# Kernel optimization log

Measured on AMD Instinct MI355X. Metric: run time of the kernel, lower is better.

The kernel has to match this reference:

```python
import jax, jax.numpy as jnp
import numpy as np


def setup_inputs() -> dict:
    key = jax.random.key(0)
    ks = jax.random.split(key, 5)
    b, t, q_dim, kv_dim, h = 16, 128, 256, 64, 4
    c = t - 1
    q_x = jax.random.normal(ks[0], (b, t, q_dim), dtype=jnp.float32)
    kv_x = jax.random.normal(ks[1], (b, t, c, kv_dim), dtype=jnp.float32)
    # Linear weights stored as [in, out]; no biases (bias=False in torch module).
    sq = 1.0 / np.sqrt(q_dim)
    sk = 1.0 / np.sqrt(kv_dim)
    Wq = jax.random.uniform(ks[2], (q_dim, kv_dim * h), jnp.float32, -sq, sq)
    Wk = jax.random.uniform(ks[3], (kv_dim, kv_dim * h), jnp.float32, -sk, sk)
    Wv = jax.random.uniform(ks[4], (kv_dim, kv_dim * h), jnp.float32, -sk, sk)
    return {"q_x": q_x, "kv_x": kv_x, "Wq": Wq, "Wk": Wk, "Wv": Wv}


def reference(q_x, kv_x, Wq, Wk, Wv):
    b, t, c, k = kv_x.shape  # c = t - 1
    h = Wq.shape[1] // k
    # projections
    q = (q_x @ Wq).reshape(b, t, h, k)          # [b,t,h,k]
    keys = (kv_x @ Wk).reshape(b, t, c, h, k)   # [b,t,c,h,k]
    vals = (kv_x @ Wv).reshape(b, t, c, h, k)
    # per-token attention over the c-sized context
    scores = jnp.einsum('bthk,btchk->bthc', q, keys) / jnp.sqrt(jnp.float32(k))
    w = jax.nn.softmax(scores, axis=-1)          # softmax over context dim
    out = jnp.einsum('bthc,btchk->bthk', w, vals)
    return out.reshape(b, t, h * k)
```

## Files before the change

### kernel.cpp

```cpp
#include <hip/hip_runtime.h>
#include <math.h>

#define Bdim 16
#define Tdim 128
#define Cdim 127
#define Hdim 4
#define QD   256
#define HK   256
#define BT   (Bdim * Tdim)

#define DPP_XOR1 0xB1
#define DPP_XOR2 0x4E
template<int CTRL>
__device__ __forceinline__ float dpp_movf(float x) {
    return __int_as_float(__builtin_amdgcn_update_dpp(
        0, __float_as_int(x), CTRL, 0xF, 0xF, true));
}
__device__ __forceinline__ float dot4(float4 a, float4 b, float s) {
    return fmaf(a.x, b.x, fmaf(a.y, b.y, fmaf(a.z, b.z, fmaf(a.w, b.w, s))));
}
__device__ __forceinline__ float4 fma4(float e, float4 x, float4 v) {
    v.x = fmaf(e, x.x, v.x); v.y = fmaf(e, x.y, v.y);
    v.z = fmaf(e, x.z, v.z); v.w = fmaf(e, x.w, v.w);
    return v;
}
__device__ __forceinline__ float4 add4(float4 a, float4 b) {
    return make_float4(a.x + b.x, a.y + b.y, a.z + b.z, a.w + b.w);
}
__device__ __forceinline__ float4 shfl4(float4 v, int m) {
    return make_float4(__shfl_xor(v.x, m, 64), __shfl_xor(v.y, m, 64),
                       __shfl_xor(v.z, m, 64), __shfl_xor(v.w, m, 64));
}
__device__ __forceinline__ float4 sel4(int c, float4 a, float4 b) {
    return c ? a : b;
}

__global__ __launch_bounds__(256) void qk_fused(
        const float* __restrict__ q_x,
        const float* __restrict__ Wq,
        const float* __restrict__ Wk,
        float* __restrict__ qk) {
    __shared__ __align__(16) float q_s[4][256];
    __shared__ __align__(16) float p_s[4][4][68];
    int RB = blockIdx.x;
    int tid = threadIdx.x;
    {
        int r = tid >> 6, kq = tid & 63;
        *(float4*)&q_s[r][kq*4] =
            *(const float4*)(q_x + (size_t)(RB*4 + r) * QD + kq * 4);
    }
    __syncthreads();

    float acc[4] = {0.f, 0.f, 0.f, 0.f};
    #pragma unroll 4
    for (int i4 = 0; i4 < 64; ++i4) {
        float w0 = Wq[(size_t)(4*i4+0) * HK + tid];
        float w1 = Wq[(size_t)(4*i4+1) * HK + tid];
        float w2 = Wq[(size_t)(4*i4+2) * HK + tid];
        float w3 = Wq[(size_t)(4*i4+3) * HK + tid];
        #pragma unroll
        for (int r = 0; r < 4; ++r) {
            float4 qv = *(const float4*)&q_s[r][i4*4];
            acc[r] = fmaf(qv.x, w0, fmaf(qv.y, w1, fmaf(qv.z, w2, fmaf(qv.w, w3, acc[r]))));
        }
    }
    int h = tid >> 6, m = tid & 63;
    #pragma unroll
    for (int r = 0; r < 4; ++r) p_s[r][h][m] = acc[r];
    __syncthreads();

    const float4* wk4 = (const float4*)(Wk + (size_t)m * HK + h * 64);
    float4 wkr[16];
    #pragma unroll
    for (int j = 0; j < 16; ++j) wkr[j] = wk4[j];
    float a2[4] = {0.f, 0.f, 0.f, 0.f};
    #pragma unroll
    for (int j4 = 0; j4 < 16; ++j4) {
        #pragma unroll
        for (int r = 0; r < 4; ++r) {
            float4 pv = *(const float4*)&p_s[r][h][j4*4];
            a2[r] = fmaf(pv.x, wkr[j4].x, fmaf(pv.y, wkr[j4].y,
                    fmaf(pv.z, wkr[j4].z, fmaf(pv.w, wkr[j4].w, a2[r]))));
        }
    }
    #pragma unroll
    for (int r = 0; r < 4; ++r)
        qk[(size_t)(RB*4 + r) * HK + tid] = a2[r];
}

__global__ __launch_bounds__(256, 4) void attn_fused(
        const float* __restrict__ kv_x,
        const float* __restrict__ qk_g,
        const float* __restrict__ Wv,
        float* __restrict__ out) {
    __shared__ __align__(16) float4 wx_s[2][4][16];
    __shared__ float dn_s[2][4];
    int tid = threadIdx.x;
    int wv = tid >> 6, lane = tid & 63;
    int slot = wv >> 1;
    int hp   = wv & 1;
    int bt = blockIdx.x * 2 + slot;
    int r  = lane >> 2;
    int jq = lane & 3;
    const float* Xr = kv_x + (size_t)bt * (Cdim * 64);

    const float4* qb = (const float4*)(qk_g + (size_t)bt * HK);
    float4 Q00 = qb[(2*hp+0)*16 + jq*4 + 0], Q01 = qb[(2*hp+0)*16 + jq*4 + 1],
           Q02 = qb[(2*hp+0)*16 + jq*4 + 2], Q03 = qb[(2*hp+0)*16 + jq*4 + 3];
    float4 Q10 = qb[(2*hp+1)*16 + jq*4 + 0], Q11 = qb[(2*hp+1)*16 + jq*4 + 1],
           Q12 = qb[(2*hp+1)*16 + jq*4 + 2], Q13 = qb[(2*hp+1)*16 + jq*4 + 3];

    float4 V00={0,0,0,0},V01={0,0,0,0},V02={0,0,0,0},V03={0,0,0,0};
    float4 V10={0,0,0,0},V11={0,0,0,0},V12={0,0,0,0},V13={0,0,0,0};
    float d0=0.f, d1=0.f;
    float4 A0, A1, A2, A3, B0, B1, B2, B3;

#define LOADR(P0,P1,P2,P3,KK) do {                                           \
    int c_ = 16*(KK) + r;                                                    \
    const float4* xp_ = (const float4*)(Xr + (size_t)((c_ < Cdim) ? c_ : 0)  \
                                        * 64) + jq * 4;                      \
    P0 = xp_[0]; P1 = xp_[1]; P2 = xp_[2]; P3 = xp_[3];                      \
} while (0)

#define COMP(P0,P1,P2,P3,KK) do {                                            \
    float s0 = dot4(Q00,P0,0.f); s0 = dot4(Q01,P1,s0);                       \
    s0 = dot4(Q02,P2,s0); s0 = dot4(Q03,P3,s0);                              \
    float s1 = dot4(Q10,P0,0.f); s1 = dot4(Q11,P1,s1);                       \
    s1 = dot4(Q12,P2,s1); s1 = dot4(Q13,P3,s1);                              \
    s0 += dpp_movf<DPP_XOR1>(s0); s0 += dpp_movf<DPP_XOR2>(s0);              \
    s1 += dpp_movf<DPP_XOR1>(s1); s1 += dpp_movf<DPP_XOR2>(s1);              \
    bool vld_ = (16*(KK) + r) < Cdim;                                        \
    float e0 = vld_ ? __expf(s0 * 0.125f) : 0.f;                             \
    float e1 = vld_ ? __expf(s1 * 0.125f) : 0.f;                             \
    d0 += e0; d1 += e1;                                                      \
    V00=fma4(e0,P0,V00); V01=fma4(e0,P1,V01);                                \
    V02=fma4(e0,P2,V02); V03=fma4(e0,P3,V03);                                \
    V10=fma4(e1,P0,V10); V11=fma4(e1,P1,V11);                                \
    V12=fma4(e1,P2,V12); V13=fma4(e1,P3,V13);                                \
} while (0)

    LOADR(A0,A1,A2,A3,0);
    LOADR(B0,B1,B2,B3,1);
    COMP (A0,A1,A2,A3,0);
    LOADR(A0,A1,A2,A3,2);
    COMP (B0,B1,B2,B3,1);
    LOADR(B0,B1,B2,B3,3);
    COMP (A0,A1,A2,A3,2);
    LOADR(A0,A1,A2,A3,4);
    COMP (B0,B1,B2,B3,3);
    LOADR(B0,B1,B2,B3,5);
    COMP (A0,A1,A2,A3,4);
    LOADR(A0,A1,A2,A3,6);
    COMP (B0,B1,B2,B3,5);
    LOADR(B0,B1,B2,B3,7);
    COMP (A0,A1,A2,A3,6);
    COMP (B0,B1,B2,B3,7);
#undef LOADR
#undef COMP

    int r0 = (lane >> 2) & 1, r1 = (lane >> 3) & 1;
    int r2 = (lane >> 4) & 1, r3 = (lane >> 5) & 1;
    float4 K00 = add4(sel4(r0, V01, V00), shfl4(sel4(r0, V00, V01), 4));
    float4 K01 = add4(sel4(r0, V03, V02), shfl4(sel4(r0, V02, V03), 4));
    float4 K10 = add4(sel4(r0, V11, V10), shfl4(sel4(r0, V10, V11), 4));
    float4 K11 = add4(sel4(r0, V13, V12), shfl4(sel4(r0, V12, V13), 4));
    float4 L0 = add4(sel4(r1, K01, K00), shfl4(sel4(r1, K00, K01), 8));
    float4 L1 = add4(sel4(r1, K11, K10), shfl4(sel4(r1, K10, K11), 8));
    float4 M = add4(sel4(r2, L1, L0), shfl4(sel4(r2, L0, L1), 16));
    float4 F = add4(M, shfl4(M, 32));

    #pragma unroll
    for (int m = 4; m <= 32; m <<= 1) {
        d0 += __shfl_xor(d0, m, 64);
        d1 += __shfl_xor(d1, m, 64);
    }

    int H  = 2*hp + r2;
    int qo = (r1 << 1) | r0;
    if (r3 == 0) wx_s[slot][H][jq * 4 + qo] = F;
    if (lane == 0) { dn_s[slot][2*hp+0] = d0; dn_s[slot][2*hp+1] = d1; }
    __syncthreads();

    #pragma unroll
    for (int s = 0; s < 2; ++s) {
        int col = tid;
        int h = col >> 6;
        float inv = 1.f / dn_s[s][h];
        const float* wvc = Wv + col;
        float acc = 0.f;
        #pragma unroll
        for (int j4 = 0; j4 < 16; ++j4) {
            float4 w4 = wx_s[s][h][j4];
            acc = fmaf(w4.x, wvc[(size_t)(j4*4+0) * HK],
                  fmaf(w4.y, wvc[(size_t)(j4*4+1) * HK],
                  fmaf(w4.z, wvc[(size_t)(j4*4+2) * HK],
                  fmaf(w4.w, wvc[(size_t)(j4*4+3) * HK], acc))));
        }
        out[(size_t)(blockIdx.x * 2 + s) * HK + col] = acc * inv;
    }
}

extern "C" void kernel_launch(void* const* d_in, const int* in_sizes, int n_in,
                              void* d_out, int out_size, void* d_ws, size_t ws_size,
                              hipStream_t stream) {
    const float* q_x  = (const float*)d_in[0];
    const float* kv_x = (const float*)d_in[1];
    const float* Wq   = (const float*)d_in[2];
    const float* Wk   = (const float*)d_in[3];
    const float* Wv   = (const float*)d_in[4];
    float* out = (float*)d_out;

    float* qk = (float*)d_ws;

    qk_fused <<<BT / 4, 256, 0, stream>>>(q_x, Wq, Wk, qk);
    attn_fused<<<BT / 2, 256, 0, stream>>>(kv_x, qk, Wv, out);
}
```

Measured before the change: 36.00 us.

## Split attention context across four waves per token, one block per token

The attention kernel now assigns one block per (b,t) token and splits the 127-row context across the four waves. Each 16-lane group covers one full row for all four heads, with a 16-lane DPP reduction, and the per-wave partials are combined in shared memory before the Wv projection. Each lane holds only four accumulator vectors, so register pressure drops and launch bounds rise to 6 blocks per CU. The cost is twice as many blocks, extra cross-wave reduction and more DPP steps per row, and each block now reads Wv for only one token instead of two.

```diff
diff --git a/kernel.cpp b/kernel.cpp
--- a/kernel.cpp
+++ b/kernel.cpp
@@ -9,8 +9,10 @@
 #define HK   256
 #define BT   (Bdim * Tdim)
 
-#define DPP_XOR1 0xB1
-#define DPP_XOR2 0x4E
+#define DPP_XOR1        0xB1
+#define DPP_XOR2        0x4E
+#define DPP_HALF_MIRROR 0x141
+#define DPP_MIRROR      0x140
 template<int CTRL>
 __device__ __forceinline__ float dpp_movf(float x) {
     return __int_as_float(__builtin_amdgcn_update_dpp(
@@ -33,6 +35,13 @@
 }
 __device__ __forceinline__ float4 sel4(int c, float4 a, float4 b) {
     return c ? a : b;
+}
+__device__ __forceinline__ float red16(float v) {
+    v += dpp_movf<DPP_XOR1>(v);
+    v += dpp_movf<DPP_XOR2>(v);
+    v += dpp_movf<DPP_HALF_MIRROR>(v);
+    v += dpp_movf<DPP_MIRROR>(v);
+    return v;
 }
 
 __global__ __launch_bounds__(256) void qk_fused(
@@ -88,115 +97,105 @@
         qk[(size_t)(RB*4 + r) * HK + tid] = a2[r];
 }
 
-__global__ __launch_bounds__(256, 4) void attn_fused(
+__global__ __launch_bounds__(256, 6) void attn_fused(
         const float* __restrict__ kv_x,
         const float* __restrict__ qk_g,
         const float* __restrict__ Wv,
         float* __restrict__ out) {
-    __shared__ __align__(16) float4 wx_s[2][4][16];
-    __shared__ float dn_s[2][4];
+    __shared__ __align__(16) float4 wx_p[4][4][16];
+    __shared__ __align__(16) float4 dn_p[4];
+
     int tid = threadIdx.x;
     int wv = tid >> 6, lane = tid & 63;
-    int slot = wv >> 1;
-    int hp   = wv & 1;
-    int bt = blockIdx.x * 2 + slot;
-    int r  = lane >> 2;
-    int jq = lane & 3;
+    int bt = blockIdx.x;
+    int rr = lane >> 4;
+    int ff = lane & 15;
+    int cbase = wv * 32;
     const float* Xr = kv_x + (size_t)bt * (Cdim * 64);
 
     const float4* qb = (const float4*)(qk_g + (size_t)bt * HK);
-    float4 Q00 = qb[(2*hp+0)*16 + jq*4 + 0], Q01 = qb[(2*hp+0)*16 + jq*4 + 1],
-           Q02 = qb[(2*hp+0)*16 + jq*4 + 2], Q03 = qb[(2*hp+0)*16 + jq*4 + 3];
-    float4 Q10 = qb[(2*hp+1)*16 + jq*4 + 0], Q11 = qb[(2*hp+1)*16 + jq*4 + 1],
-           Q12 = qb[(2*hp+1)*16 + jq*4 + 2], Q13 = qb[(2*hp+1)*16 + jq*4 + 3];
-
-    float4 V00={0,0,0,0},V01={0,0,0,0},V02={0,0,0,0},V03={0,0,0,0};
-    float4 V10={0,0,0,0},V11={0,0,0,0},V12={0,0,0,0},V13={0,0,0,0};
-    float d0=0.f, d1=0.f;
-    float4 A0, A1, A2, A3, B0, B1, B2, B3;
-
-#define LOADR(P0,P1,P2,P3,KK) do {                                           \
-    int c_ = 16*(KK) + r;                                                    \
-    const float4* xp_ = (const float4*)(Xr + (size_t)((c_ < Cdim) ? c_ : 0)  \
-                                        * 64) + jq * 4;                      \
-    P0 = xp_[0]; P1 = xp_[1]; P2 = xp_[2]; P3 = xp_[3];                      \
+    float4 Q0 = qb[0*16 + ff], Q1 = qb[1*16 + ff],
+           Q2 = qb[2*16 + ff], Q3 = qb[3*16 + ff];
+
+    float4 V0 = {0,0,0,0}, V1 = {0,0,0,0}, V2 = {0,0,0,0}, V3 = {0,0,0,0};
+    float d0 = 0.f, d1 = 0.f, d2 = 0.f, d3 = 0.f;
+    float4 A, B, C, D;
+
+#define LOADP(P,KK) do {                                                     \
+    int c_ = cbase + 4*(KK) + rr;                                            \
+    P = *((const float4*)(Xr + (size_t)((c_ < Cdim) ? c_ : 0) * 64) + ff);   \
 } while (0)
 
-#define COMP(P0,P1,P2,P3,KK) do {                                            \
-    float s0 = dot4(Q00,P0,0.f); s0 = dot4(Q01,P1,s0);                       \
-    s0 = dot4(Q02,P2,s0); s0 = dot4(Q03,P3,s0);                              \
-    float s1 = dot4(Q10,P0,0.f); s1 = dot4(Q11,P1,s1);                       \
-    s1 = dot4(Q12,P2,s1); s1 = dot4(Q13,P3,s1);                              \
-    s0 += dpp_movf<DPP_XOR1>(s0); s0 += dpp_movf<DPP_XOR2>(s0);              \
-    s1 += dpp_movf<DPP_XOR1>(s1); s1 += dpp_movf<DPP_XOR2>(s1);              \
-    bool vld_ = (16*(KK) + r) < Cdim;                                        \
+#define COMP(P,KK) do {                                                      \
+    float s0 = dot4(Q0, P, 0.f);                                             \
+    float s1 = dot4(Q1, P, 0.f);                                             \
+    float s2 = dot4(Q2, P, 0.f);                                             \
+    float s3 = dot4(Q3, P, 0.f);                                             \
+    s0 = red16(s0); s1 = red16(s1); s2 = red16(s2); s3 = red16(s3);          \
+    bool vld_ = (cbase + 4*(KK) + rr) < Cdim;                                \
     float e0 = vld_ ? __expf(s0 * 0.125f) : 0.f;                             \
     float e1 = vld_ ? __expf(s1 * 0.125f) : 0.f;                             \
-    d0 += e0; d1 += e1;                                                      \
-    V00=fma4(e0,P0,V00); V01=fma4(e0,P1,V01);                                \
-    V02=fma4(e0,P2,V02); V03=fma4(e0,P3,V03);                                \
-    V10=fma4(e1,P0,V10); V11=fma4(e1,P1,V11);                                \
-    V12=fma4(e1,P2,V12); V13=fma4(e1,P3,V13);                                \
+    float e2 = vld_ ? __expf(s2 * 0.125f) : 0.f;                             \
+    float e3 = vld_ ? __expf(s3 * 0.125f) : 0.f;                             \
+    d0 += e0; d1 += e1; d2 += e2; d3 += e3;                                  \
+    V0 = fma4(e0, P, V0); V1 = fma4(e1, P, V1);                              \
+    V2 = fma4(e2, P, V2); V3 = fma4(e3, P, V3);                              \
 } while (0)
 
-    LOADR(A0,A1,A2,A3,0);
-    LOADR(B0,B1,B2,B3,1);
-    COMP (A0,A1,A2,A3,0);
-    LOADR(A0,A1,A2,A3,2);
-    COMP (B0,B1,B2,B3,1);
-    LOADR(B0,B1,B2,B3,3);
-    COMP (A0,A1,A2,A3,2);
-    LOADR(A0,A1,A2,A3,4);
-    COMP (B0,B1,B2,B3,3);
-    LOADR(B0,B1,B2,B3,5);
-    COMP (A0,A1,A2,A3,4);
-    LOADR(A0,A1,A2,A3,6);
-    COMP (B0,B1,B2,B3,5);
-    LOADR(B0,B1,B2,B3,7);
-    COMP (A0,A1,A2,A3,6);
-    COMP (B0,B1,B2,B3,7);
-#undef LOADR
+    LOADP(A,0);
+    LOADP(B,1);
+    LOADP(C,2);
+    LOADP(D,3);
+    COMP (A,0);
+    LOADP(A,4);
+    COMP (B,1);
+    LOADP(B,5);
+    COMP (C,2);
+    LOADP(C,6);
+    COMP (D,3);
+    LOADP(D,7);
+    COMP (A,4);
+    COMP (B,5);
+    COMP (C,6);
+    COMP (D,7);
+#undef LOADP
 #undef COMP
 
-    int r0 = (lane >> 2) & 1, r1 = (lane >> 3) & 1;
-    int r2 = (lane >> 4) & 1, r3 = (lane >> 5) & 1;
-    float4 K00 = add4(sel4(r0, V01, V00), shfl4(sel4(r0, V00, V01), 4));
-    float4 K01 = add4(sel4(r0, V03, V02), shfl4(sel4(r0, V02, V03), 4));
-    float4 K10 = add4(sel4(r0, V11, V10), shfl4(sel4(r0, V10, V11), 4));
-    float4 K11 = add4(sel4(r0, V13, V12), shfl4(sel4(r0, V12, V13), 4));
-    float4 L0 = add4(sel4(r1, K01, K00), shfl4(sel4(r1, K00, K01), 8));
-    float4 L1 = add4(sel4(r1, K11, K10), shfl4(sel4(r1, K10, K11), 8));
-    float4 M = add4(sel4(r2, L1, L0), shfl4(sel4(r2, L0, L1), 16));
-    float4 F = add4(M, shfl4(M, 32));
-
-    #pragma unroll
-    for (int m = 4; m <= 32; m <<= 1) {
-        d0 += __shfl_xor(d0, m, 64);
-        d1 += __shfl_xor(d1, m, 64);
-    }
-
-    int H  = 2*hp + r2;
-    int qo = (r1 << 1) | r0;
-    if (r3 == 0) wx_s[slot][H][jq * 4 + qo] = F;
-    if (lane == 0) { dn_s[slot][2*hp+0] = d0; dn_s[slot][2*hp+1] = d1; }
+    int r4 = (lane >> 4) & 1, r5 = (lane >> 5) & 1;
+    float4 G0 = add4(sel4(r4, V1, V0), shfl4(sel4(r4, V0, V1), 16));
+    float4 G1 = add4(sel4(r4, V3, V2), shfl4(sel4(r4, V2, V3), 16));
+    float4 F  = add4(sel4(r5, G1, G0), shfl4(sel4(r5, G0, G1), 32));
+    int H = (r5 << 1) | r4;
+    wx_p[wv][H][ff] = F;
+
+    d0 += __shfl_xor(d0, 16, 64); d0 += __shfl_xor(d0, 32, 64);
+    d1 += __shfl_xor(d1, 16, 64); d1 += __shfl_xor(d1, 32, 64);
+    d2 += __shfl_xor(d2, 16, 64); d2 += __shfl_xor(d2, 32, 64);
+    d3 += __shfl_xor(d3, 16, 64); d3 += __shfl_xor(d3, 32, 64);
+    if (lane == 0) dn_p[wv] = make_float4(d0, d1, d2, d3);
     __syncthreads();
 
-    #pragma unroll
-    for (int s = 0; s < 2; ++s) {
-        int col = tid;
-        int h = col >> 6;
-        float inv = 1.f / dn_s[s][h];
+    {
+        int h = tid >> 6, col = tid;
+        float4 n0 = dn_p[0], n1 = dn_p[1], n2 = dn_p[2], n3 = dn_p[3];
+        float4 ns = make_float4(n0.x+n1.x+n2.x+n3.x, n0.y+n1.y+n2.y+n3.y,
+                                n0.z+n1.z+n2.z+n3.z, n0.w+n1.w+n2.w+n3.w);
+        float dn = (h == 0) ? ns.x : (h == 1) ? ns.y
+                 : (h == 2) ? ns.z : ns.w;
+        float inv = 1.f / dn;
         const float* wvc = Wv + col;
         float acc = 0.f;
         #pragma unroll
-        for (int j4 = 0; j4 < 16; ++j4) {
-            float4 w4 = wx_s[s][h][j4];
-            acc = fmaf(w4.x, wvc[(size_t)(j4*4+0) * HK],
-                  fmaf(w4.y, wvc[(size_t)(j4*4+1) * HK],
-                  fmaf(w4.z, wvc[(size_t)(j4*4+2) * HK],
-                  fmaf(w4.w, wvc[(size_t)(j4*4+3) * HK], acc))));
+        for (int f4 = 0; f4 < 16; ++f4) {
+            float4 w = add4(add4(wx_p[0][h][f4], wx_p[1][h][f4]),
+                            add4(wx_p[2][h][f4], wx_p[3][h][f4]));
+            int j = f4 * 4;
+            acc = fmaf(w.x, wvc[(size_t)(j+0) * HK],
+                  fmaf(w.y, wvc[(size_t)(j+1) * HK],
+                  fmaf(w.z, wvc[(size_t)(j+2) * HK],
+                  fmaf(w.w, wvc[(size_t)(j+3) * HK], acc))));
         }
-        out[(size_t)(blockIdx.x * 2 + s) * HK + col] = acc * inv;
+        out[(size_t)bt * HK + col] = acc * inv;
     }
 }
 
@@ -213,5 +212,5 @@
     float* qk = (float*)d_ws;
 
     qk_fused <<<BT / 4, 256, 0, stream>>>(q_x, Wq, Wk, qk);
-    attn_fused<<<BT / 2, 256, 0, stream>>>(kv_x, qk, Wv, out);
-}
+    attn_fused<<<BT, 256, 0, stream>>>(kv_x, qk, Wv, out);
+}
```

New measurement: 46.95 us. 30.4% more time.

## Prefetch second half of kv context rows into LDS via async global_load_lds

Applied to the files above, without the earlier changes.

At kernel start, each attention block issues asynchronous global-to-LDS loads for context rows 64..126 of its two tokens, storing them with an XOR swizzle to avoid bank conflicts. The first half of the rows is still streamed through registers. The second half is then read from LDS after a block barrier. The aim is to put more memory requests in flight early so that part of the HBM latency on the dominant kv_x stream is hidden. In exchange, each block uses 32KB of extra LDS, which may limit occupancy, and correctness depends on the barrier waiting for the async loads to finish.

```diff
diff --git a/kernel.cpp b/kernel.cpp
--- a/kernel.cpp
+++ b/kernel.cpp
@@ -93,8 +93,10 @@
         const float* __restrict__ qk_g,
         const float* __restrict__ Wv,
         float* __restrict__ out) {
+    __shared__ __align__(16) float4 sX[2][64 * 16];
     __shared__ __align__(16) float4 wx_s[2][4][16];
     __shared__ float dn_s[2][4];
+
     int tid = threadIdx.x;
     int wv = tid >> 6, lane = tid & 63;
     int slot = wv >> 1;
@@ -103,6 +105,18 @@
     int r  = lane >> 2;
     int jq = lane & 3;
     const float* Xr = kv_x + (size_t)bt * (Cdim * 64);
+    const float4* Xr4 = (const float4*)Xr;
+
+    #pragma unroll
+    for (int t = 0; t < 8; ++t) {
+        int l = hp * 512 + t * 64 + lane;
+        int c = 64 + (l >> 4), p = l & 15;
+        int csrc = (c < Cdim) ? c : (Cdim - 1);
+        __builtin_amdgcn_global_load_lds(
+            (const __attribute__((address_space(1))) void*)
+                (Xr4 + (size_t)csrc * 16 + (p ^ (c & 7))),
+            (__attribute__((address_space(3))) void*)(&sX[slot][l]), 16, 0, 0);
+    }
 
     const float4* qb = (const float4*)(qk_g + (size_t)bt * HK);
     float4 Q00 = qb[(2*hp+0)*16 + jq*4 + 0], Q01 = qb[(2*hp+0)*16 + jq*4 + 1],
@@ -116,10 +130,19 @@
     float4 A0, A1, A2, A3, B0, B1, B2, B3;
 
 #define LOADR(P0,P1,P2,P3,KK) do {                                           \
-    int c_ = 16*(KK) + r;                                                    \
-    const float4* xp_ = (const float4*)(Xr + (size_t)((c_ < Cdim) ? c_ : 0)  \
-                                        * 64) + jq * 4;                      \
+    int c_ = 16*(KK) + r;                            \
+    const float4* xp_ = Xr4 + (size_t)c_ * 16 + jq * 4;                      \
     P0 = xp_[0]; P1 = xp_[1]; P2 = xp_[2]; P3 = xp_[3];                      \
+} while (0)
+
+#define LOADL(P0,P1,P2,P3,KK) do {                                           \
+    int c_ = 16*(KK) + r;                                       \
+    const float4* lb_ = &sX[slot][(c_ - 64) * 16];                           \
+    int sw_ = c_ & 7;                                            \
+    P0 = lb_[(jq*4 + 0) ^ sw_];                                              \
+    P1 = lb_[(jq*4 + 1) ^ sw_];                                              \
+    P2 = lb_[(jq*4 + 2) ^ sw_];                                              \
+    P3 = lb_[(jq*4 + 3) ^ sw_];                                              \
 } while (0)
 
 #define COMP(P0,P1,P2,P3,KK) do {                                            \
@@ -146,16 +169,20 @@
     COMP (B0,B1,B2,B3,1);
     LOADR(B0,B1,B2,B3,3);
     COMP (A0,A1,A2,A3,2);
-    LOADR(A0,A1,A2,A3,4);
     COMP (B0,B1,B2,B3,3);
-    LOADR(B0,B1,B2,B3,5);
+
+    __syncthreads();
+
+    LOADL(A0,A1,A2,A3,4);
+    LOADL(B0,B1,B2,B3,5);
     COMP (A0,A1,A2,A3,4);
-    LOADR(A0,A1,A2,A3,6);
+    LOADL(A0,A1,A2,A3,6);
     COMP (B0,B1,B2,B3,5);
-    LOADR(B0,B1,B2,B3,7);
+    LOADL(B0,B1,B2,B3,7);
     COMP (A0,A1,A2,A3,6);
     COMP (B0,B1,B2,B3,7);
 #undef LOADR
+#undef LOADL
 #undef COMP
 
     int r0 = (lane >> 2) & 1, r1 = (lane >> 3) & 1;
```

Result: slower. 36.87 us (+2.4%).
